# Performance work log

Measured on AMD Instinct MI355X. Metric: run time of the kernel, lower is better.

The kernel has to match this reference:

```python
import jax, jax.numpy as jnp
import numpy as np

N_NODES = 50000
N_EDGES = 800000
IN_DIM = 128
OUT_DIM = 64


def setup_inputs() -> dict:
    key = jax.random.key(0)
    k1, k2, k3, k4, k5, k6 = jax.random.split(key, 6)
    x = jax.random.normal(k1, (N_NODES, IN_DIM), dtype=jnp.float32)
    edge_row = jax.random.randint(k2, (N_EDGES,), 0, N_NODES, dtype=jnp.int32)
    edge_col = jax.random.randint(k3, (N_EDGES,), 0, N_NODES, dtype=jnp.int32)
    edge_val = jax.random.uniform(k4, (N_EDGES,), dtype=jnp.float32)
    stdv = 1.0 / np.sqrt(OUT_DIM)
    w = jax.random.uniform(k5, (IN_DIM, OUT_DIM), minval=-stdv, maxval=stdv, dtype=jnp.float32)
    b = jax.random.uniform(k6, (OUT_DIM,), minval=-stdv, maxval=stdv, dtype=jnp.float32)
    return {"x": x, "edge_row": edge_row, "edge_col": edge_col, "edge_val": edge_val, "w": w, "b": b}


def reference(x, edge_row, edge_col, edge_val, w, b):
    # dense projection: [N, in_dim] @ [in_dim, out_dim] -> [N, out_dim]
    hidden = x @ w
    # SpMM: out[r] = sum_e val[e] * hidden[col[e]] for edges with row[e] == r
    msg = hidden[edge_col] * edge_val[:, None]          # [E, out_dim]
    out = jax.ops.segment_sum(msg, edge_row, num_segments=N_NODES)
    return jax.nn.relu(out + b)
```

## Files before the change

### kernel.cpp

```cpp
#include <hip/hip_runtime.h>

#define N_NODES 50000
#define N_EDGES 800000
#define IN_DIM 128
#define OUT_DIM 64
#define CAP 64
#define PARTS 8
#define ROWS_PER_PART 6250
#define EDGES_PER_CHUNK 3125

#define OFF_HID 0u
#define OFF_DEG 6400000u
#define OFF_BKT 6600192u

typedef short short8 __attribute__((ext_vector_type(8)));
typedef float f32x4 __attribute__((ext_vector_type(4)));

__device__ __forceinline__ unsigned short bf_rne(float f) {
    unsigned u = __float_as_uint(f);
    u += 0x7fffu + ((u >> 16) & 1u);
    return (unsigned short)(u >> 16);
}
__device__ __forceinline__ float bf_lo(unsigned u) { return __uint_as_float(u << 16); }
__device__ __forceinline__ float bf_hi(unsigned u) { return __uint_as_float(u & 0xffff0000u); }

__global__ __launch_bounds__(256) void gemm_kernel(const float* __restrict__ x,
                                                   const float* __restrict__ w,
                                                   unsigned short* __restrict__ hidb) {
    __shared__ unsigned short wperm[16 * 64 * 8];
    __shared__ unsigned short obuf[4][16 * 64];

    const int tid = threadIdx.x;
    const int lane = tid & 63;
    const int wid = tid >> 6;

    for (int s = tid; s < 16 * 64 * 8; s += 256) {
        const int f = s >> 9;
        const int ln = (s >> 3) & 63;
        const int j = s & 7;
        const int c = f >> 2, t = f & 3;
        const int k = c * 32 + (ln >> 4) * 8 + j;
        const int n = t * 16 + (ln & 15);
        wperm[s] = bf_rne(w[k * OUT_DIM + n]);
    }
    __syncthreads();

    const int group = blockIdx.x * 4 + wid;
    if (group < N_NODES / 16) {
        short8 bf[16];
        #pragma unroll
        for (int f = 0; f < 16; ++f)
            bf[f] = *(const short8*)&wperm[(f * 64 + lane) * 8];

        const int node0 = group * 16;
        f32x4 acc[4] = {{0, 0, 0, 0}, {0, 0, 0, 0}, {0, 0, 0, 0}, {0, 0, 0, 0}};

        #pragma unroll
        for (int c = 0; c < 4; ++c) {
            const float* xr = x + (size_t)(node0 + (lane & 15)) * IN_DIM + c * 32 + (lane >> 4) * 8;
            const float4 a0 = *(const float4*)xr;
            const float4 a1 = *(const float4*)(xr + 4);
            short8 af;
            af[0] = (short)bf_rne(a0.x); af[1] = (short)bf_rne(a0.y);
            af[2] = (short)bf_rne(a0.z); af[3] = (short)bf_rne(a0.w);
            af[4] = (short)bf_rne(a1.x); af[5] = (short)bf_rne(a1.y);
            af[6] = (short)bf_rne(a1.z); af[7] = (short)bf_rne(a1.w);
            #pragma unroll
            for (int t = 0; t < 4; ++t)
                acc[t] = __builtin_amdgcn_mfma_f32_16x16x32_bf16(af, bf[c * 4 + t], acc[t], 0, 0, 0);
        }

        #pragma unroll
        for (int t = 0; t < 4; ++t)
            #pragma unroll
            for (int r = 0; r < 4; ++r)
                obuf[wid][((lane >> 4) * 4 + r) * 64 + t * 16 + (lane & 15)] = bf_rne(acc[t][r]);
        const uint4 o0 = *(const uint4*)&obuf[wid][lane * 16];
        const uint4 o1 = *(const uint4*)&obuf[wid][lane * 16 + 8];
        char* dst = (char*)hidb + (size_t)node0 * (OUT_DIM * 2) + lane * 32;
        *(uint4*)dst = o0;
        *(uint4*)(dst + 16) = o1;
    }
}

__global__ __launch_bounds__(256) void bucket_kernel(const int* __restrict__ erow,
                                                     const int* __restrict__ ecol,
                                                     const float* __restrict__ eval,
                                                     int* __restrict__ deg,
                                                     int2* __restrict__ bucket) {
    const int part = blockIdx.x & (PARTS - 1);
    const int chunk = blockIdx.x >> 3;
    const int rlo = part * ROWS_PER_PART;
    const int e0 = chunk * EDGES_PER_CHUNK;
    for (int i = threadIdx.x; i < EDGES_PER_CHUNK; i += 256) {
        const int e = e0 + i;
        const int r = erow[e];
        const int c = ecol[e];
        const float v = eval[e];
        if ((unsigned)(r - rlo) < (unsigned)ROWS_PER_PART) {
            const int pos = atomicAdd(&deg[r], 1);
            if (pos < CAP) bucket[(size_t)r * CAP + pos] = make_int2(c, __float_as_int(v));
        }
    }
}

__global__ __launch_bounds__(256) void agg_kernel(const unsigned short* __restrict__ hidb,
                                                  const int* __restrict__ deg,
                                                  const int2* __restrict__ bucket,
                                                  const float* __restrict__ b,
                                                  float* __restrict__ out) {
    const int g = blockIdx.x * 4 + (threadIdx.x >> 6);
    const int lane = threadIdx.x & 63;
    const int half = lane >> 5;
    const int l = lane & 31;
    const int row = g * 2 + half;
    if (row >= N_NODES) return;

    const int d = min(deg[row], CAP);
    const int2* __restrict__ ep = bucket + (size_t)row * CAP;

    float acc0 = 0.f, acc1 = 0.f;
    int i = 0;
    for (; i + 4 <= d; i += 4) {
        const int2 p0 = ep[i], p1 = ep[i + 1], p2 = ep[i + 2], p3 = ep[i + 3];
        const unsigned u0 = *(const unsigned*)&hidb[(size_t)p0.x * OUT_DIM + 2 * l];
        const unsigned u1 = *(const unsigned*)&hidb[(size_t)p1.x * OUT_DIM + 2 * l];
        const unsigned u2 = *(const unsigned*)&hidb[(size_t)p2.x * OUT_DIM + 2 * l];
        const unsigned u3 = *(const unsigned*)&hidb[(size_t)p3.x * OUT_DIM + 2 * l];
        const float v0 = __int_as_float(p0.y), v1 = __int_as_float(p1.y);
        const float v2 = __int_as_float(p2.y), v3 = __int_as_float(p3.y);
        acc0 = fmaf(v0, bf_lo(u0), acc0); acc1 = fmaf(v0, bf_hi(u0), acc1);
        acc0 = fmaf(v1, bf_lo(u1), acc0); acc1 = fmaf(v1, bf_hi(u1), acc1);
        acc0 = fmaf(v2, bf_lo(u2), acc0); acc1 = fmaf(v2, bf_hi(u2), acc1);
        acc0 = fmaf(v3, bf_lo(u3), acc0); acc1 = fmaf(v3, bf_hi(u3), acc1);
    }
    for (; i < d; ++i) {
        const int2 p = ep[i];
        const unsigned u = *(const unsigned*)&hidb[(size_t)p.x * OUT_DIM + 2 * l];
        const float v = __int_as_float(p.y);
        acc0 = fmaf(v, bf_lo(u), acc0); acc1 = fmaf(v, bf_hi(u), acc1);
    }
    const float2 bb = *(const float2*)&b[2 * l];
    float2 o;
    o.x = fmaxf(acc0 + bb.x, 0.f);
    o.y = fmaxf(acc1 + bb.y, 0.f);
    *(float2*)&out[(size_t)row * OUT_DIM + 2 * l] = o;
}

extern "C" void kernel_launch(void* const* d_in, const int* in_sizes, int n_in,
                              void* d_out, int out_size, void* d_ws, size_t ws_size,
                              hipStream_t stream) {
    const float* x    = (const float*)d_in[0];
    const int*   erow = (const int*)d_in[1];
    const int*   ecol = (const int*)d_in[2];
    const float* eval = (const float*)d_in[3];
    const float* w    = (const float*)d_in[4];
    const float* b    = (const float*)d_in[5];
    float* out = (float*)d_out;

    char* ws = (char*)d_ws;
    unsigned short* hidb = (unsigned short*)(ws + OFF_HID);
    int*  deg    = (int*)(ws + OFF_DEG);
    int2* bucket = (int2*)(ws + OFF_BKT);

    hipMemsetAsync(deg, 0, N_NODES * sizeof(int), stream);

    gemm_kernel<<<(N_NODES / 16 + 3) / 4, 256, 0, stream>>>(x, w, hidb);

    bucket_kernel<<<256 * PARTS, 256, 0, stream>>>(erow, ecol, eval, deg, bucket);

    agg_kernel<<<(N_NODES / 2 + 3) / 4, 256, 0, stream>>>(hidb, deg, bucket, b, out);
}
```

Measured before the change: 157.2 us.

## Fuse GEMM with edge bucketing and shard buckets into per-section sub-buckets

```diff
diff --git a/kernel.cpp b/kernel.cpp
--- a/kernel.cpp
+++ b/kernel.cpp
@@ -4,14 +4,16 @@
 #define N_EDGES 800000
 #define IN_DIM 128
 #define OUT_DIM 64
-#define CAP 64
-#define PARTS 8
-#define ROWS_PER_PART 6250
-#define EDGES_PER_CHUNK 3125
+#define SECTIONS 8
+#define SCAP 24
+#define N_TILES (N_EDGES / 64)
+#define GEMM_GROUPS (N_NODES / 16)
+#define GEMM_BLOCKS ((GEMM_GROUPS + 3) / 4)
 
 #define OFF_HID 0u
-#define OFF_DEG 6400000u
-#define OFF_BKT 6600192u
+#define OFF_CTR 6400000u
+#define OFF_DEG 6400064u
+#define OFF_BKT 8000064u
 
 typedef short short8 __attribute__((ext_vector_type(8)));
 typedef float f32x4 __attribute__((ext_vector_type(4)));
@@ -21,12 +23,16 @@
     u += 0x7fffu + ((u >> 16) & 1u);
     return (unsigned short)(u >> 16);
 }
-__device__ __forceinline__ float bf_lo(unsigned u) { return __uint_as_float(u << 16); }
-__device__ __forceinline__ float bf_hi(unsigned u) { return __uint_as_float(u & 0xffff0000u); }
+__device__ __forceinline__ float bf_load(const unsigned short* p) {
+    return __uint_as_float(((unsigned)*p) << 16);
+}
 
-__global__ __launch_bounds__(256) void gemm_kernel(const float* __restrict__ x,
-                                                   const float* __restrict__ w,
-                                                   unsigned short* __restrict__ hidb) {
+__global__ __launch_bounds__(256) void gemm_bucket_kernel(
+        const float* __restrict__ x, const float* __restrict__ w,
+        const int* __restrict__ erow, const int* __restrict__ ecol,
+        const float* __restrict__ eval,
+        unsigned short* __restrict__ hidb, int* __restrict__ ctr,
+        int* __restrict__ deg8, int2* __restrict__ bucket8) {
     __shared__ unsigned short wperm[16 * 64 * 8];
     __shared__ unsigned short obuf[4][16 * 64];
 
@@ -34,117 +40,123 @@
     const int lane = tid & 63;
     const int wid = tid >> 6;
 
-    for (int s = tid; s < 16 * 64 * 8; s += 256) {
-        const int f = s >> 9;
-        const int ln = (s >> 3) & 63;
-        const int j = s & 7;
-        const int c = f >> 2, t = f & 3;
-        const int k = c * 32 + (ln >> 4) * 8 + j;
-        const int n = t * 16 + (ln & 15);
-        wperm[s] = bf_rne(w[k * OUT_DIM + n]);
-    }
-    __syncthreads();
+    if (blockIdx.x < GEMM_BLOCKS) {
+        for (int s = tid; s < 16 * 64 * 8; s += 256) {
+            const int f = s >> 9;
+            const int ln = (s >> 3) & 63;
+            const int j = s & 7;
+            const int c = f >> 2, t = f & 3;
+            const int k = c * 32 + (ln >> 4) * 8 + j;
+            const int n = t * 16 + (ln & 15);
+            wperm[s] = bf_rne(w[k * OUT_DIM + n]);
+        }
+        __syncthreads();
 
-    const int group = blockIdx.x * 4 + wid;
-    if (group < N_NODES / 16) {
-        short8 bf[16];
-        #pragma unroll
-        for (int f = 0; f < 16; ++f)
-            bf[f] = *(const short8*)&wperm[(f * 64 + lane) * 8];
+        const int group = blockIdx.x * 4 + wid;
+        if (group < GEMM_GROUPS) {
+            short8 bfr[16];
+            #pragma unroll
+            for (int f = 0; f < 16; ++f)
+                bfr[f] = *(const short8*)&wperm[(f * 64 + lane) * 8];
 
-        const int node0 = group * 16;
-        f32x4 acc[4] = {{0, 0, 0, 0}, {0, 0, 0, 0}, {0, 0, 0, 0}, {0, 0, 0, 0}};
+            const int node0 = group * 16;
+            f32x4 acc[4] = {{0, 0, 0, 0}, {0, 0, 0, 0}, {0, 0, 0, 0}, {0, 0, 0, 0}};
 
-        #pragma unroll
-        for (int c = 0; c < 4; ++c) {
-            const float* xr = x + (size_t)(node0 + (lane & 15)) * IN_DIM + c * 32 + (lane >> 4) * 8;
-            const float4 a0 = *(const float4*)xr;
-            const float4 a1 = *(const float4*)(xr + 4);
-            short8 af;
-            af[0] = (short)bf_rne(a0.x); af[1] = (short)bf_rne(a0.y);
-            af[2] = (short)bf_rne(a0.z); af[3] = (short)bf_rne(a0.w);
-            af[4] = (short)bf_rne(a1.x); af[5] = (short)bf_rne(a1.y);
-            af[6] = (short)bf_rne(a1.z); af[7] = (short)bf_rne(a1.w);
+            #pragma unroll
+            for (int c = 0; c < 4; ++c) {
+                const float* xr = x + (size_t)(node0 + (lane & 15)) * IN_DIM + c * 32 + (lane >> 4) * 8;
+                const float4 a0 = *(const float4*)xr;
+                const float4 a1 = *(const float4*)(xr + 4);
+                short8 af;
+                af[0] = (short)bf_rne(a0.x); af[1] = (short)bf_rne(a0.y);
+                af[2] = (short)bf_rne(a0.z); af[3] = (short)bf_rne(a0.w);
+                af[4] = (short)bf_rne(a1.x); af[5] = (short)bf_rne(a1.y);
+                af[6] = (short)bf_rne(a1.z); af[7] = (short)bf_rne(a1.w);
+                #pragma unroll
+                for (int t = 0; t < 4; ++t)
+                    acc[t] = __builtin_amdgcn_mfma_f32_16x16x32_bf16(af, bfr[c * 4 + t], acc[t], 0, 0, 0);
+            }
             #pragma unroll
             for (int t = 0; t < 4; ++t)
-                acc[t] = __builtin_amdgcn_mfma_f32_16x16x32_bf16(af, bf[c * 4 + t], acc[t], 0, 0, 0);
+                #pragma unroll
+                for (int r = 0; r < 4; ++r)
+                    obuf[wid][((lane >> 4) * 4 + r) * 64 + t * 16 + (lane & 15)] = bf_rne(acc[t][r]);
+            const uint4 o0 = *(const uint4*)&obuf[wid][lane * 16];
+            const uint4 o1 = *(const uint4*)&obuf[wid][lane * 16 + 8];
+            char* dst = (char*)hidb + (size_t)node0 * (OUT_DIM * 2) + lane * 32;
+            *(uint4*)dst = o0;
+            *(uint4*)(dst + 16) = o1;
         }
+    }
 
-        #pragma unroll
-        for (int t = 0; t < 4; ++t)
-            #pragma unroll
-            for (int r = 0; r < 4; ++r)
-                obuf[wid][((lane >> 4) * 4 + r) * 64 + t * 16 + (lane & 15)] = bf_rne(acc[t][r]);
-        const uint4 o0 = *(const uint4*)&obuf[wid][lane * 16];
-        const uint4 o1 = *(const uint4*)&obuf[wid][lane * 16 + 8];
-        char* dst = (char*)hidb + (size_t)node0 * (OUT_DIM * 2) + lane * 32;
-        *(uint4*)dst = o0;
-        *(uint4*)(dst + 16) = o1;
-    }
-}
-
-__global__ __launch_bounds__(256) void bucket_kernel(const int* __restrict__ erow,
-                                                     const int* __restrict__ ecol,
-                                                     const float* __restrict__ eval,
-                                                     int* __restrict__ deg,
-                                                     int2* __restrict__ bucket) {
-    const int part = blockIdx.x & (PARTS - 1);
-    const int chunk = blockIdx.x >> 3;
-    const int rlo = part * ROWS_PER_PART;
-    const int e0 = chunk * EDGES_PER_CHUNK;
-    for (int i = threadIdx.x; i < EDGES_PER_CHUNK; i += 256) {
-        const int e = e0 + i;
+    const int sec = blockIdx.x & (SECTIONS - 1);
+    int* __restrict__ mydeg = deg8 + sec * N_NODES;
+    int2* __restrict__ mybkt = bucket8 + (size_t)sec * N_NODES * SCAP;
+    for (;;) {
+        int t = 0;
+        if (lane == 0) t = atomicAdd(ctr, 1);
+        t = __shfl(t, 0);
+        if (t >= N_TILES) break;
+        const int e = t * 64 + lane;
         const int r = erow[e];
         const int c = ecol[e];
         const float v = eval[e];
-        if ((unsigned)(r - rlo) < (unsigned)ROWS_PER_PART) {
-            const int pos = atomicAdd(&deg[r], 1);
-            if (pos < CAP) bucket[(size_t)r * CAP + pos] = make_int2(c, __float_as_int(v));
-        }
+        const int pos = atomicAdd(&mydeg[r], 1);
+        if (pos < SCAP) mybkt[(size_t)r * SCAP + pos] = make_int2(c, __float_as_int(v));
     }
 }
 
 __global__ __launch_bounds__(256) void agg_kernel(const unsigned short* __restrict__ hidb,
-                                                  const int* __restrict__ deg,
-                                                  const int2* __restrict__ bucket,
+                                                  const int* __restrict__ deg8,
+                                                  const int2* __restrict__ bucket8,
                                                   const float* __restrict__ b,
                                                   float* __restrict__ out) {
-    const int g = blockIdx.x * 4 + (threadIdx.x >> 6);
+    const int row = blockIdx.x * 4 + (threadIdx.x >> 6);
     const int lane = threadIdx.x & 63;
-    const int half = lane >> 5;
-    const int l = lane & 31;
-    const int row = g * 2 + half;
     if (row >= N_NODES) return;
 
-    const int d = min(deg[row], CAP);
-    const int2* __restrict__ ep = bucket + (size_t)row * CAP;
+    int cum[9];
+    cum[0] = 0;
+    #pragma unroll
+    for (int s = 0; s < 8; ++s) {
+        const int d = min(deg8[s * N_NODES + row], SCAP);
+        cum[s + 1] = cum[s] + d;
+    }
+    const int total = min(cum[8], 64);
 
-    float acc0 = 0.f, acc1 = 0.f;
-    int i = 0;
-    for (; i + 4 <= d; i += 4) {
-        const int2 p0 = ep[i], p1 = ep[i + 1], p2 = ep[i + 2], p3 = ep[i + 3];
-        const unsigned u0 = *(const unsigned*)&hidb[(size_t)p0.x * OUT_DIM + 2 * l];
-        const unsigned u1 = *(const unsigned*)&hidb[(size_t)p1.x * OUT_DIM + 2 * l];
-        const unsigned u2 = *(const unsigned*)&hidb[(size_t)p2.x * OUT_DIM + 2 * l];
-        const unsigned u3 = *(const unsigned*)&hidb[(size_t)p3.x * OUT_DIM + 2 * l];
-        const float v0 = __int_as_float(p0.y), v1 = __int_as_float(p1.y);
-        const float v2 = __int_as_float(p2.y), v3 = __int_as_float(p3.y);
-        acc0 = fmaf(v0, bf_lo(u0), acc0); acc1 = fmaf(v0, bf_hi(u0), acc1);
-        acc0 = fmaf(v1, bf_lo(u1), acc0); acc1 = fmaf(v1, bf_hi(u1), acc1);
-        acc0 = fmaf(v2, bf_lo(u2), acc0); acc1 = fmaf(v2, bf_hi(u2), acc1);
-        acc0 = fmaf(v3, bf_lo(u3), acc0); acc1 = fmaf(v3, bf_hi(u3), acc1);
+    int ec = 0, ev = 0;
+    if (lane < total) {
+        int sec = 0;
+        #pragma unroll
+        for (int s = 1; s < 8; ++s) sec += (lane >= cum[s]);
+        const int idx = lane - cum[sec];
+        const int2 p = bucket8[((size_t)(sec * N_NODES + row)) * SCAP + idx];
+        ec = p.x;
+        ev = p.y;
     }
-    for (; i < d; ++i) {
-        const int2 p = ep[i];
-        const unsigned u = *(const unsigned*)&hidb[(size_t)p.x * OUT_DIM + 2 * l];
-        const float v = __int_as_float(p.y);
-        acc0 = fmaf(v, bf_lo(u), acc0); acc1 = fmaf(v, bf_hi(u), acc1);
+
+    float acc = 0.f;
+    int t = 0;
+    for (; t + 4 <= total; t += 4) {
+        const int c0 = __shfl(ec, t), c1 = __shfl(ec, t + 1);
+        const int c2 = __shfl(ec, t + 2), c3 = __shfl(ec, t + 3);
+        const int w0 = __shfl(ev, t), w1 = __shfl(ev, t + 1);
+        const int w2 = __shfl(ev, t + 2), w3 = __shfl(ev, t + 3);
+        const float h0 = bf_load(&hidb[(size_t)c0 * OUT_DIM + lane]);
+        const float h1 = bf_load(&hidb[(size_t)c1 * OUT_DIM + lane]);
+        const float h2 = bf_load(&hidb[(size_t)c2 * OUT_DIM + lane]);
+        const float h3 = bf_load(&hidb[(size_t)c3 * OUT_DIM + lane]);
+        acc = fmaf(__int_as_float(w0), h0, acc);
+        acc = fmaf(__int_as_float(w1), h1, acc);
+        acc = fmaf(__int_as_float(w2), h2, acc);
+        acc = fmaf(__int_as_float(w3), h3, acc);
     }
-    const float2 bb = *(const float2*)&b[2 * l];
-    float2 o;
-    o.x = fmaxf(acc0 + bb.x, 0.f);
-    o.y = fmaxf(acc1 + bb.y, 0.f);
-    *(float2*)&out[(size_t)row * OUT_DIM + 2 * l] = o;
+    for (; t < total; ++t) {
+        const int c = __shfl(ec, t);
+        const int wv = __shfl(ev, t);
+        acc = fmaf(__int_as_float(wv), bf_load(&hidb[(size_t)c * OUT_DIM + lane]), acc);
+    }
+    out[(size_t)row * OUT_DIM + lane] = fmaxf(acc + b[lane], 0.f);
 }
 
 extern "C" void kernel_launch(void* const* d_in, const int* in_sizes, int n_in,
@@ -160,14 +172,14 @@
 
     char* ws = (char*)d_ws;
     unsigned short* hidb = (unsigned short*)(ws + OFF_HID);
-    int*  deg    = (int*)(ws + OFF_DEG);
-    int2* bucket = (int2*)(ws + OFF_BKT);
+    int*  ctr     = (int*)(ws + OFF_CTR);
+    int*  deg8    = (int*)(ws + OFF_DEG);
+    int2* bucket8 = (int2*)(ws + OFF_BKT);
 
-    hipMemsetAsync(deg, 0, N_NODES * sizeof(int), stream);
+    hipMemsetAsync(ws + OFF_CTR, 0, 64 + SECTIONS * N_NODES * sizeof(int), stream);
 
-    gemm_kernel<<<(N_NODES / 16 + 3) / 4, 256, 0, stream>>>(x, w, hidb);
+    gemm_bucket_kernel<<<2048, 256, 0, stream>>>(x, w, erow, ecol, eval,
+                                                 hidb, ctr, deg8, bucket8);
 
-    bucket_kernel<<<256 * PARTS, 256, 0, stream>>>(erow, ecol, eval, deg, bucket);
-
-    agg_kernel<<<(N_NODES / 2 + 3) / 4, 256, 0, stream>>>(hidb, deg, bucket, b, out);
+    agg_kernel<<<(N_NODES + 3) / 4, 256, 0, stream>>>(hidb, deg8, bucket8, b, out);
 }
```

Measured after the change: 359.3 us. 129% more time.

## Fuse GEMM and edge bucketing into one launch, precompute permuted weights

Applied to the files above, without the earlier changes.

```diff
diff --git a/kernel.cpp b/kernel.cpp
--- a/kernel.cpp
+++ b/kernel.cpp
@@ -5,13 +5,15 @@
 #define IN_DIM 128
 #define OUT_DIM 64
 #define CAP 64
-#define PARTS 8
-#define ROWS_PER_PART 6250
-#define EDGES_PER_CHUNK 3125
+
+#define GEMM_GROUPS (N_NODES / 16)
+#define GEMM_BLOCKS ((GEMM_GROUPS + 3) / 4)
+#define BUCKET_BLOCKS (N_EDGES / 256)
 
 #define OFF_HID 0u
 #define OFF_DEG 6400000u
-#define OFF_BKT 6600192u
+#define OFF_WP  6600192u
+#define OFF_BKT 6616576u
 
 typedef short short8 __attribute__((ext_vector_type(8)));
 typedef float f32x4 __attribute__((ext_vector_type(4)));
@@ -24,84 +26,77 @@
 __device__ __forceinline__ float bf_lo(unsigned u) { return __uint_as_float(u << 16); }
 __device__ __forceinline__ float bf_hi(unsigned u) { return __uint_as_float(u & 0xffff0000u); }
 
-__global__ __launch_bounds__(256) void gemm_kernel(const float* __restrict__ x,
-                                                   const float* __restrict__ w,
-                                                   unsigned short* __restrict__ hidb) {
-    __shared__ unsigned short wperm[16 * 64 * 8];
-    __shared__ unsigned short obuf[4][16 * 64];
+__global__ __launch_bounds__(256) void wprep_kernel(const float* __restrict__ w,
+                                                    unsigned short* __restrict__ wperm) {
+    const int s = blockIdx.x * 256 + threadIdx.x;
+    const int f = s >> 9;
+    const int ln = (s >> 3) & 63;
+    const int j = s & 7;
+    const int c = f >> 2, t = f & 3;
+    const int k = c * 32 + (ln >> 4) * 8 + j;
+    const int n = t * 16 + (ln & 15);
+    wperm[s] = bf_rne(w[k * OUT_DIM + n]);
+}
 
+__global__ __launch_bounds__(256) void gemm_bucket_kernel(
+        const float* __restrict__ x, const unsigned short* __restrict__ wperm,
+        const int* __restrict__ erow, const int* __restrict__ ecol,
+        const float* __restrict__ eval,
+        unsigned short* __restrict__ hidb,
+        int* __restrict__ deg, int2* __restrict__ bucket) {
     const int tid = threadIdx.x;
     const int lane = tid & 63;
     const int wid = tid >> 6;
 
-    for (int s = tid; s < 16 * 64 * 8; s += 256) {
-        const int f = s >> 9;
-        const int ln = (s >> 3) & 63;
-        const int j = s & 7;
-        const int c = f >> 2, t = f & 3;
-        const int k = c * 32 + (ln >> 4) * 8 + j;
-        const int n = t * 16 + (ln & 15);
-        wperm[s] = bf_rne(w[k * OUT_DIM + n]);
-    }
-    __syncthreads();
-
-    const int group = blockIdx.x * 4 + wid;
-    if (group < N_NODES / 16) {
-        short8 bf[16];
-        #pragma unroll
-        for (int f = 0; f < 16; ++f)
-            bf[f] = *(const short8*)&wperm[(f * 64 + lane) * 8];
-
-        const int node0 = group * 16;
-        f32x4 acc[4] = {{0, 0, 0, 0}, {0, 0, 0, 0}, {0, 0, 0, 0}, {0, 0, 0, 0}};
-
-        #pragma unroll
-        for (int c = 0; c < 4; ++c) {
-            const float* xr = x + (size_t)(node0 + (lane & 15)) * IN_DIM + c * 32 + (lane >> 4) * 8;
-            const float4 a0 = *(const float4*)xr;
-            const float4 a1 = *(const float4*)(xr + 4);
-            short8 af;
-            af[0] = (short)bf_rne(a0.x); af[1] = (short)bf_rne(a0.y);
-            af[2] = (short)bf_rne(a0.z); af[3] = (short)bf_rne(a0.w);
-            af[4] = (short)bf_rne(a1.x); af[5] = (short)bf_rne(a1.y);
-            af[6] = (short)bf_rne(a1.z); af[7] = (short)bf_rne(a1.w);
-            #pragma unroll
-            for (int t = 0; t < 4; ++t)
-                acc[t] = __builtin_amdgcn_mfma_f32_16x16x32_bf16(af, bf[c * 4 + t], acc[t], 0, 0, 0);
-        }
-
-        #pragma unroll
-        for (int t = 0; t < 4; ++t)
-            #pragma unroll
-            for (int r = 0; r < 4; ++r)
-                obuf[wid][((lane >> 4) * 4 + r) * 64 + t * 16 + (lane & 15)] = bf_rne(acc[t][r]);
-        const uint4 o0 = *(const uint4*)&obuf[wid][lane * 16];
-        const uint4 o1 = *(const uint4*)&obuf[wid][lane * 16 + 8];
-        char* dst = (char*)hidb + (size_t)node0 * (OUT_DIM * 2) + lane * 32;
-        *(uint4*)dst = o0;
-        *(uint4*)(dst + 16) = o1;
-    }
-}
-
-__global__ __launch_bounds__(256) void bucket_kernel(const int* __restrict__ erow,
-                                                     const int* __restrict__ ecol,
-                                                     const float* __restrict__ eval,
-                                                     int* __restrict__ deg,
-                                                     int2* __restrict__ bucket) {
-    const int part = blockIdx.x & (PARTS - 1);
-    const int chunk = blockIdx.x >> 3;
-    const int rlo = part * ROWS_PER_PART;
-    const int e0 = chunk * EDGES_PER_CHUNK;
-    for (int i = threadIdx.x; i < EDGES_PER_CHUNK; i += 256) {
-        const int e = e0 + i;
+    if (blockIdx.x >= GEMM_BLOCKS) {
+        const int e = (blockIdx.x - GEMM_BLOCKS) * 256 + tid;
         const int r = erow[e];
         const int c = ecol[e];
         const float v = eval[e];
-        if ((unsigned)(r - rlo) < (unsigned)ROWS_PER_PART) {
-            const int pos = atomicAdd(&deg[r], 1);
-            if (pos < CAP) bucket[(size_t)r * CAP + pos] = make_int2(c, __float_as_int(v));
-        }
+        const int pos = atomicAdd(&deg[r], 1);
+        if (pos < CAP) bucket[(size_t)r * CAP + pos] = make_int2(c, __float_as_int(v));
+        return;
     }
+
+    __shared__ unsigned short obuf[4][16 * 64];
+
+    const int group = blockIdx.x * 4 + wid;
+    if (group >= GEMM_GROUPS) return;
+
+    const short8* wp = (const short8*)wperm;
+    short8 bfr[16];
+    #pragma unroll
+    for (int f = 0; f < 16; ++f)
+        bfr[f] = wp[f * 64 + lane];
+
+    const int node0 = group * 16;
+    f32x4 acc[4] = {{0, 0, 0, 0}, {0, 0, 0, 0}, {0, 0, 0, 0}, {0, 0, 0, 0}};
+
+    #pragma unroll
+    for (int c = 0; c < 4; ++c) {
+        const float* xr = x + (size_t)(node0 + (lane & 15)) * IN_DIM + c * 32 + (lane >> 4) * 8;
+        const float4 a0 = *(const float4*)xr;
+        const float4 a1 = *(const float4*)(xr + 4);
+        short8 af;
+        af[0] = (short)bf_rne(a0.x); af[1] = (short)bf_rne(a0.y);
+        af[2] = (short)bf_rne(a0.z); af[3] = (short)bf_rne(a0.w);
+        af[4] = (short)bf_rne(a1.x); af[5] = (short)bf_rne(a1.y);
+        af[6] = (short)bf_rne(a1.z); af[7] = (short)bf_rne(a1.w);
+        #pragma unroll
+        for (int t = 0; t < 4; ++t)
+            acc[t] = __builtin_amdgcn_mfma_f32_16x16x32_bf16(af, bfr[c * 4 + t], acc[t], 0, 0, 0);
+    }
+
+    #pragma unroll
+    for (int t = 0; t < 4; ++t)
+        #pragma unroll
+        for (int r = 0; r < 4; ++r)
+            obuf[wid][((lane >> 4) * 4 + r) * 64 + t * 16 + (lane & 15)] = bf_rne(acc[t][r]);
+    const uint4 o0 = *(const uint4*)&obuf[wid][lane * 16];
+    const uint4 o1 = *(const uint4*)&obuf[wid][lane * 16 + 8];
+    char* dst = (char*)hidb + (size_t)node0 * (OUT_DIM * 2) + lane * 32;
+    *(uint4*)dst = o0;
+    *(uint4*)(dst + 16) = o1;
 }
 
 __global__ __launch_bounds__(256) void agg_kernel(const unsigned short* __restrict__ hidb,
@@ -159,15 +154,17 @@
     float* out = (float*)d_out;
 
     char* ws = (char*)d_ws;
-    unsigned short* hidb = (unsigned short*)(ws + OFF_HID);
-    int*  deg    = (int*)(ws + OFF_DEG);
-    int2* bucket = (int2*)(ws + OFF_BKT);
+    unsigned short* hidb  = (unsigned short*)(ws + OFF_HID);
+    int*            deg   = (int*)(ws + OFF_DEG);
+    unsigned short* wperm = (unsigned short*)(ws + OFF_WP);
+    int2*           bucket = (int2*)(ws + OFF_BKT);
 
     hipMemsetAsync(deg, 0, N_NODES * sizeof(int), stream);
 
-    gemm_kernel<<<(N_NODES / 16 + 3) / 4, 256, 0, stream>>>(x, w, hidb);
+    wprep_kernel<<<32, 256, 0, stream>>>(w, wperm);
 
-    bucket_kernel<<<256 * PARTS, 256, 0, stream>>>(erow, ecol, eval, deg, bucket);
+    gemm_bucket_kernel<<<GEMM_BLOCKS + BUCKET_BLOCKS, 256, 0, stream>>>(
+        x, wperm, erow, ecol, eval, hidb, deg, bucket);
 
     agg_kernel<<<(N_NODES / 2 + 3) / 4, 256, 0, stream>>>(hidb, deg, bucket, b, out);
 }
```

After: 171.5 us. +9.1%, slower.
